# Kernel tuning notes

Measured on AMD Instinct MI355X. Metric: run time of the kernel, lower is better.

## Reference

```python
import jax, jax.numpy as jnp
import numpy as np

N_SRC1, N_DST1, N_DST2 = 200000, 50000, 10000
E1, E2 = 2000000, 400000
IN_F, H_F, N_CLS = 128, 256, 47


def setup_inputs() -> dict:
    key = jax.random.key(0)
    ks = jax.random.split(key, 10)
    x = jax.random.normal(ks[0], (N_SRC1, IN_F), dtype=jnp.float32)
    W_self1 = jax.random.normal(ks[1], (IN_F, H_F), dtype=jnp.float32) * (1.0 / np.sqrt(IN_F))
    W_neigh1 = jax.random.normal(ks[2], (IN_F, H_F), dtype=jnp.float32) * (1.0 / np.sqrt(IN_F))
    b1 = jnp.zeros((H_F,), dtype=jnp.float32)
    W_self2 = jax.random.normal(ks[3], (H_F, N_CLS), dtype=jnp.float32) * (1.0 / np.sqrt(H_F))
    W_neigh2 = jax.random.normal(ks[4], (H_F, N_CLS), dtype=jnp.float32) * (1.0 / np.sqrt(H_F))
    b2 = jnp.zeros((N_CLS,), dtype=jnp.float32)
    src1 = jax.random.randint(ks[5], (E1,), 0, N_SRC1, dtype=jnp.int64)
    dst1 = jnp.sort(jax.random.randint(ks[6], (E1,), 0, N_DST1, dtype=jnp.int64))
    src2 = jax.random.randint(ks[7], (E2,), 0, N_DST1, dtype=jnp.int64)
    dst2 = jnp.sort(jax.random.randint(ks[8], (E2,), 0, N_DST2, dtype=jnp.int64))
    return {"x": x, "W_self1": W_self1, "W_neigh1": W_neigh1, "b1": b1,
            "W_self2": W_self2, "W_neigh2": W_neigh2, "b2": b2,
            "src1": src1, "dst1": dst1, "src2": src2, "dst2": dst2,
            "n_dst1": N_DST1, "n_dst2": N_DST2}


def _sage_mean(h_src, h_dst, src, dst, n_dst, W_self, W_neigh, b):
    # mean neighbor aggregation: gather src feats, segment-sum onto dst, divide by in-degree
    msum = jax.ops.segment_sum(h_src[src], dst, num_segments=n_dst)  # [n_dst, F]
    deg = jax.ops.segment_sum(jnp.ones(src.shape, h_src.dtype), dst, num_segments=n_dst)
    h_neigh = msum / jnp.maximum(deg, 1.0)[:, None]
    return h_dst @ W_self + h_neigh @ W_neigh + b


def reference(x, W_self1, W_neigh1, b1, W_self2, W_neigh2, b2,
              src1, dst1, src2, dst2, n_dst1, n_dst2):
    # layer 1 (dst nodes are the prefix of src nodes, DGL MFG convention)
    h = _sage_mean(x, x[:n_dst1], src1, dst1, n_dst1, W_self1, W_neigh1, b1)
    h = jax.nn.relu(h)  # dropout = identity (eval mode)
    # layer 2
    out = _sage_mean(h, h[:n_dst2], src2, dst2, n_dst2, W_self2, W_neigh2, b2)
    return out
```

## Files before the change

### kernel.cpp

```cpp
#include <hip/hip_runtime.h>

constexpr int N_DST1 = 50000;
constexpr int N_DST2 = 10000;
constexpr int E1     = 2000000;
constexpr int E2     = 400000;
constexpr int IN_F   = 128;
constexpr int H_F    = 256;
constexpr int N_CLS  = 47;

constexpr size_t RP1_OFF = 0;
constexpr size_t RP2_OFF = 204800;
constexpr size_t BPS_OFF = 245760;
constexpr size_t BPN_OFF = 311296;
constexpr size_t BP2_OFF = 376832;
constexpr size_t X8_OFF  = 430080;
constexpr size_t HN1_OFF = 26030080;
constexpr size_t HB_OFF  = 38830080;
constexpr size_t H8_OFF  = 64430080;
constexpr size_t HN2_OFF = 77230080;

using f32x4  = __attribute__((ext_vector_type(4))) float;
using f32x2  = __attribute__((ext_vector_type(2))) float;
using short8 = __attribute__((ext_vector_type(8))) short;

__device__ __forceinline__ ushort f2bf(float f) {
    union { float f; unsigned u; } v; v.f = f;
    unsigned u = v.u;
    return (ushort)((u + 0x7fffu + ((u >> 16) & 1u)) >> 16);
}

constexpr int CAST_BLKS = 200000 * IN_F / 8 / 256;
constexpr int PACK_BLKS = 44;
constexpr int RP_BLKS   = (N_DST1 + N_DST2 + 2 + 255) / 256;

__global__ __launch_bounds__(256) void setup_all(
    const float* __restrict__ x, unsigned char* __restrict__ x8,
    const float* __restrict__ Ws1, const float* __restrict__ Wn1,
    const float* __restrict__ Ws2, const float* __restrict__ Wn2,
    ushort* __restrict__ bps, ushort* __restrict__ bpn, ushort* __restrict__ bp2,
    const int* __restrict__ dst1, const int* __restrict__ dst2,
    int* __restrict__ rp1, int* __restrict__ rp2) {
    int b = blockIdx.x;
    if (b < CAST_BLKS) {
        int i = b * 256 + threadIdx.x;
        float4 v0 = ((const float4*)x)[2 * i];
        float4 v1 = ((const float4*)x)[2 * i + 1];
        int p0 = __builtin_amdgcn_cvt_pk_fp8_f32(v0.x, v0.y, 0, false);
        p0     = __builtin_amdgcn_cvt_pk_fp8_f32(v0.z, v0.w, p0, true);
        int p1 = __builtin_amdgcn_cvt_pk_fp8_f32(v1.x, v1.y, 0, false);
        p1     = __builtin_amdgcn_cvt_pk_fp8_f32(v1.z, v1.w, p1, true);
        uint2 o; o.x = (unsigned)p0; o.y = (unsigned)p1;
        ((uint2*)x8)[i] = o;
    } else if (b < CAST_BLKS + PACK_BLKS) {
        int pb = b - CAST_BLKS;
        if (pb < 32) {
            const float* W = (pb < 16) ? Ws1 : Wn1;
            ushort* P      = (pb < 16) ? bps : bpn;
            int idx = (pb & 15) * 256 + threadIdx.x;
            int lane = idx & 63, kb = (idx >> 6) & 3, nb = idx >> 8;
            int n  = nb * 16 + (lane & 15);
            int k0 = kb * 32 + ((lane >> 4) * 8);
            ushort tmp[8];
#pragma unroll
            for (int j = 0; j < 8; ++j) tmp[j] = f2bf(W[(k0 + j) * H_F + n]);
            ((uint4*)P)[idx] = *(uint4*)tmp;
        } else {
            int idx = (pb - 32) * 256 + threadIdx.x;
            if (idx < 3072) {
                int lane = idx & 63, rem = idx >> 6;
                int nb = rem % 3, kb = rem / 3;
                int col = nb * 16 + (lane & 15);
                int k0  = (kb & 7) * 32 + ((lane >> 4) * 8);
                const float* W = (kb < 8) ? Ws2 : Wn2;
                ushort tmp[8];
#pragma unroll
                for (int j = 0; j < 8; ++j)
                    tmp[j] = (col < N_CLS) ? f2bf(W[(k0 + j) * N_CLS + col]) : (ushort)0;
                ((uint4*)bp2)[(kb * 3 + nb) * 64 + lane] = *(uint4*)tmp;
            }
        }
    } else {
        int idx = (b - CAST_BLKS - PACK_BLKS) * 256 + threadIdx.x;
        const int* dst; int* rp; int E; int target;
        if (idx <= N_DST1) { dst = dst1; rp = rp1; E = E1; target = idx; }
        else if (idx <= N_DST1 + 1 + N_DST2) {
            dst = dst2; rp = rp2; E = E2; target = idx - (N_DST1 + 1);
        } else return;
        int lo = 0, hi = E;
        while (lo < hi) {
            int mid = (lo + hi) >> 1;
            if (dst[mid] < target) lo = mid + 1; else hi = mid;
        }
        rp[target] = lo;
    }
}

__global__ __launch_bounds__(256) void agg1b(const unsigned char* __restrict__ x8,
                                             const int* __restrict__ src,
                                             const int* __restrict__ rp,
                                             ushort* __restrict__ hn) {
    int t = threadIdx.x & 63;
    int d = blockIdx.x * 4 + (threadIdx.x >> 6);
    int s = rp[d], e = rp[d + 1];
    int deg = e - s;
    const uint4* x4 = (const uint4*)x8;
    int g = t >> 3, c = t & 7;
    float a[16] = {};
    auto acc16 = [&](uint4 v) {
        f32x2 f;
        f = __builtin_amdgcn_cvt_pk_f32_fp8((int)v.x, false); a[0]  += f[0]; a[1]  += f[1];
        f = __builtin_amdgcn_cvt_pk_f32_fp8((int)v.x, true);  a[2]  += f[0]; a[3]  += f[1];
        f = __builtin_amdgcn_cvt_pk_f32_fp8((int)v.y, false); a[4]  += f[0]; a[5]  += f[1];
        f = __builtin_amdgcn_cvt_pk_f32_fp8((int)v.y, true);  a[6]  += f[0]; a[7]  += f[1];
        f = __builtin_amdgcn_cvt_pk_f32_fp8((int)v.z, false); a[8]  += f[0]; a[9]  += f[1];
        f = __builtin_amdgcn_cvt_pk_f32_fp8((int)v.z, true);  a[10] += f[0]; a[11] += f[1];
        f = __builtin_amdgcn_cvt_pk_f32_fp8((int)v.w, false); a[12] += f[0]; a[13] += f[1];
        f = __builtin_amdgcn_cvt_pk_f32_fp8((int)v.w, true);  a[14] += f[0]; a[15] += f[1];
    };
    int nfull = deg >> 3;
    int j = 0;
    for (; j + 2 <= nfull; j += 2) {
        int e0 = src[s + 8 * j + g];
        int e1 = src[s + 8 * j + 8 + g];
        uint4 v0 = x4[(size_t)e0 * 8 + c];
        uint4 v1 = x4[(size_t)e1 * 8 + c];
        acc16(v0);
        acc16(v1);
    }
    for (; j < nfull; ++j) {
        int e0 = src[s + 8 * j + g];
        uint4 v = x4[(size_t)e0 * 8 + c];
        acc16(v);
    }
    int b0 = s + 8 * nfull;
    int n = e - b0;
    if (g < n) {
        int e0 = src[b0 + g];
        uint4 v = x4[(size_t)e0 * 8 + c];
        acc16(v);
    }
#pragma unroll
    for (int q = 0; q < 16; ++q) {
        a[q] += __shfl_xor(a[q], 8);
        a[q] += __shfl_xor(a[q], 16);
        a[q] += __shfl_xor(a[q], 32);
    }
    if (t < 8) {
        float inv = 1.f / fmaxf((float)deg, 1.f);
        unsigned o[8];
#pragma unroll
        for (int p = 0; p < 8; ++p)
            o[p] = (unsigned)f2bf(a[2 * p] * inv) |
                   ((unsigned)f2bf(a[2 * p + 1] * inv) << 16);
        uint4* hrow = (uint4*)hn + (size_t)d * 16 + t * 2;
        hrow[0] = make_uint4(o[0], o[1], o[2], o[3]);
        hrow[1] = make_uint4(o[4], o[5], o[6], o[7]);
    }
}

__global__ __launch_bounds__(256) void agg2b(const unsigned char* __restrict__ h8,
                                             const int* __restrict__ src,
                                             const int* __restrict__ rp,
                                             ushort* __restrict__ hn) {
    int t = threadIdx.x & 63;
    int d = blockIdx.x * 4 + (threadIdx.x >> 6);
    int s = rp[d], e = rp[d + 1];
    int deg = e - s;
    const uint4* h4 = (const uint4*)h8;
    int g = t >> 4, c = t & 15;
    float a[16] = {};
    auto acc16 = [&](uint4 v) {
        f32x2 f;
        f = __builtin_amdgcn_cvt_pk_f32_fp8((int)v.x, false); a[0]  += f[0]; a[1]  += f[1];
        f = __builtin_amdgcn_cvt_pk_f32_fp8((int)v.x, true);  a[2]  += f[0]; a[3]  += f[1];
        f = __builtin_amdgcn_cvt_pk_f32_fp8((int)v.y, false); a[4]  += f[0]; a[5]  += f[1];
        f = __builtin_amdgcn_cvt_pk_f32_fp8((int)v.y, true);  a[6]  += f[0]; a[7]  += f[1];
        f = __builtin_amdgcn_cvt_pk_f32_fp8((int)v.z, false); a[8]  += f[0]; a[9]  += f[1];
        f = __builtin_amdgcn_cvt_pk_f32_fp8((int)v.z, true);  a[10] += f[0]; a[11] += f[1];
        f = __builtin_amdgcn_cvt_pk_f32_fp8((int)v.w, false); a[12] += f[0]; a[13] += f[1];
        f = __builtin_amdgcn_cvt_pk_f32_fp8((int)v.w, true);  a[14] += f[0]; a[15] += f[1];
    };
    int nfull = deg >> 2;
    int j = 0;
    for (; j + 2 <= nfull; j += 2) {
        int e0 = src[s + 4 * j + g];
        int e1 = src[s + 4 * j + 4 + g];
        uint4 v0 = h4[(size_t)e0 * 16 + c];
        uint4 v1 = h4[(size_t)e1 * 16 + c];
        acc16(v0);
        acc16(v1);
    }
    for (; j < nfull; ++j) {
        int e0 = src[s + 4 * j + g];
        uint4 v = h4[(size_t)e0 * 16 + c];
        acc16(v);
    }
    int b0 = s + 4 * nfull;
    int n = e - b0;
    if (g < n) {
        int e0 = src[b0 + g];
        uint4 v = h4[(size_t)e0 * 16 + c];
        acc16(v);
    }
#pragma unroll
    for (int q = 0; q < 16; ++q) {
        a[q] += __shfl_xor(a[q], 16);
        a[q] += __shfl_xor(a[q], 32);
    }
    if (t < 16) {
        float inv = 1.f / fmaxf((float)deg, 1.f);
        unsigned o[8];
#pragma unroll
        for (int p = 0; p < 8; ++p)
            o[p] = (unsigned)f2bf(a[2 * p] * inv) |
                   ((unsigned)f2bf(a[2 * p + 1] * inv) << 16);
        uint4* hrow = (uint4*)hn + (size_t)d * 32 + t * 2;
        hrow[0] = make_uint4(o[0], o[1], o[2], o[3]);
        hrow[1] = make_uint4(o[4], o[5], o[6], o[7]);
    }
}

__global__ __launch_bounds__(256) void gemm1_mfma(
    const float* __restrict__ x, const ushort* __restrict__ hn1,
    const ushort* __restrict__ BpS, const ushort* __restrict__ BpN,
    const float* __restrict__ b1, ushort* __restrict__ hb,
    unsigned char* __restrict__ h8) {
    int tid = threadIdx.x;
    int wave = tid >> 6, lane = tid & 63;
    int m0 = blockIdx.x * 16;
    int nb0 = wave * 4;
    int mloc = lane & 15;
    int mrow = m0 + mloc;
    int koff = (lane >> 4) * 8;

    const float*  Af = x   + (size_t)mrow * IN_F;
    const ushort* Ah = hn1 + (size_t)mrow * IN_F;
    short8 a0[4], a1[4];
#pragma unroll
    for (int kb = 0; kb < 4; ++kb) {
        float4 q0 = *(const float4*)(Af + kb * 32 + koff);
        float4 q1 = *(const float4*)(Af + kb * 32 + koff + 4);
        a0[kb][0] = (short)f2bf(q0.x); a0[kb][1] = (short)f2bf(q0.y);
        a0[kb][2] = (short)f2bf(q0.z); a0[kb][3] = (short)f2bf(q0.w);
        a0[kb][4] = (short)f2bf(q1.x); a0[kb][5] = (short)f2bf(q1.y);
        a0[kb][6] = (short)f2bf(q1.z); a0[kb][7] = (short)f2bf(q1.w);
        a1[kb] = *(const short8*)(Ah + kb * 32 + koff);
    }

    f32x4 acc[4];
#pragma unroll
    for (int nb = 0; nb < 4; ++nb) acc[nb] = (f32x4){0.f, 0.f, 0.f, 0.f};

#pragma unroll
    for (int kb = 0; kb < 4; ++kb)
#pragma unroll
        for (int nb = 0; nb < 4; ++nb) {
            short8 b = *(const short8*)(BpS + ((size_t)((nb0 + nb) * 4 + kb) * 64 + lane) * 8);
            acc[nb] = __builtin_amdgcn_mfma_f32_16x16x32_bf16(a0[kb], b, acc[nb], 0, 0, 0);
        }
#pragma unroll
    for (int kb = 0; kb < 4; ++kb)
#pragma unroll
        for (int nb = 0; nb < 4; ++nb) {
            short8 b = *(const short8*)(BpN + ((size_t)((nb0 + nb) * 4 + kb) * 64 + lane) * 8);
            acc[nb] = __builtin_amdgcn_mfma_f32_16x16x32_bf16(a1[kb], b, acc[nb], 0, 0, 0);
        }

    int crow0 = m0 + (lane >> 4) * 4;
    int ccol  = lane & 15;
#pragma unroll
    for (int nb = 0; nb < 4; ++nb) {
        size_t col = (size_t)(nb0 + nb) * 16 + ccol;
        float bias = b1[col];
#pragma unroll
        for (int r = 0; r < 4; ++r) {
            int row = crow0 + r;
            float v = fmaxf(acc[nb][r] + bias, 0.f);
            int p = __builtin_amdgcn_cvt_pk_fp8_f32(v, v, 0, false);
            h8[(size_t)row * H_F + col] = (unsigned char)(p & 0xff);
            if (row < N_DST2) hb[(size_t)row * H_F + col] = f2bf(v);
        }
    }
}

__global__ __launch_bounds__(256) void gemm2_mfma(
    const ushort* __restrict__ hb, const ushort* __restrict__ hn2,
    const ushort* __restrict__ P2, const float* __restrict__ b2,
    float* __restrict__ out) {
    int tid = threadIdx.x;
    int wave = tid >> 6, lane = tid & 63;
    int m0 = (blockIdx.x * 4 + wave) * 16;
    if (m0 >= N_DST2) return;
    int mrow = m0 + (lane & 15);
    int koff = (lane >> 4) * 8;

    f32x4 acc[3];
#pragma unroll
    for (int nb = 0; nb < 3; ++nb) acc[nb] = (f32x4){0.f, 0.f, 0.f, 0.f};

#pragma unroll
    for (int kb = 0; kb < 16; ++kb) {
        const ushort* A = (kb < 8)
            ? (hb  + (size_t)mrow * H_F + kb * 32 + koff)
            : (hn2 + (size_t)mrow * H_F + (kb - 8) * 32 + koff);
        short8 a = *(const short8*)A;
#pragma unroll
        for (int nb = 0; nb < 3; ++nb) {
            short8 b = *(const short8*)(P2 + ((size_t)(kb * 3 + nb) * 64 + lane) * 8);
            acc[nb] = __builtin_amdgcn_mfma_f32_16x16x32_bf16(a, b, acc[nb], 0, 0, 0);
        }
    }
    int crow0 = m0 + (lane >> 4) * 4;
    int ccol  = lane & 15;
#pragma unroll
    for (int nb = 0; nb < 3; ++nb) {
        int col = nb * 16 + ccol;
        if (col < N_CLS) {
            float bias = b2[col];
#pragma unroll
            for (int r = 0; r < 4; ++r)
                out[(size_t)(crow0 + r) * N_CLS + col] = acc[nb][r] + bias;
        }
    }
}

extern "C" void kernel_launch(void* const* d_in, const int* in_sizes, int n_in,
                              void* d_out, int out_size, void* d_ws, size_t ws_size,
                              hipStream_t stream) {
    const float* x   = (const float*)d_in[0];
    const float* Ws1 = (const float*)d_in[1];
    const float* Wn1 = (const float*)d_in[2];
    const float* b1  = (const float*)d_in[3];
    const float* Ws2 = (const float*)d_in[4];
    const float* Wn2 = (const float*)d_in[5];
    const float* b2  = (const float*)d_in[6];
    const int* src1  = (const int*)d_in[7];
    const int* dst1  = (const int*)d_in[8];
    const int* src2  = (const int*)d_in[9];
    const int* dst2  = (const int*)d_in[10];
    float* out = (float*)d_out;

    char* ws = (char*)d_ws;
    int*           rp1 = (int*)(ws + RP1_OFF);
    int*           rp2 = (int*)(ws + RP2_OFF);
    ushort*        bps = (ushort*)(ws + BPS_OFF);
    ushort*        bpn = (ushort*)(ws + BPN_OFF);
    ushort*        bp2 = (ushort*)(ws + BP2_OFF);
    unsigned char* x8  = (unsigned char*)(ws + X8_OFF);
    ushort*        hn1 = (ushort*)(ws + HN1_OFF);
    ushort*        hb  = (ushort*)(ws + HB_OFF);
    unsigned char* h8  = (unsigned char*)(ws + H8_OFF);
    ushort*        hn2 = (ushort*)(ws + HN2_OFF);

    setup_all<<<CAST_BLKS + PACK_BLKS + RP_BLKS, 256, 0, stream>>>(
        x, x8, Ws1, Wn1, Ws2, Wn2, bps, bpn, bp2, dst1, dst2, rp1, rp2);
    agg1b<<<N_DST1 / 4, 256, 0, stream>>>(x8, src1, rp1, hn1);
    gemm1_mfma<<<N_DST1 / 16, 256, 0, stream>>>(x, hn1, bps, bpn, b1, hb, h8);
    agg2b<<<N_DST2 / 4, 256, 0, stream>>>(h8, src2, rp2, hn2);
    gemm2_mfma<<<(N_DST2 / 16 + 3) / 4, 256, 0, stream>>>(hb, hn2, bp2, b2, out);
}
```

Before: 287.6 us.

## Fuse neighbor aggregation into GEMM kernels via LDS staging, split-K in layer two

```diff
diff --git a/kernel.cpp b/kernel.cpp
--- a/kernel.cpp
+++ b/kernel.cpp
@@ -14,10 +14,8 @@
 constexpr size_t BPN_OFF = 311296;
 constexpr size_t BP2_OFF = 376832;
 constexpr size_t X8_OFF  = 430080;
-constexpr size_t HN1_OFF = 26030080;
 constexpr size_t HB_OFF  = 38830080;
 constexpr size_t H8_OFF  = 64430080;
-constexpr size_t HN2_OFF = 77230080;
 
 using f32x4  = __attribute__((ext_vector_type(4))) float;
 using f32x2  = __attribute__((ext_vector_type(2))) float;
@@ -95,146 +93,85 @@
     }
 }
 
-__global__ __launch_bounds__(256) void agg1b(const unsigned char* __restrict__ x8,
-                                             const int* __restrict__ src,
-                                             const int* __restrict__ rp,
-                                             ushort* __restrict__ hn) {
-    int t = threadIdx.x & 63;
-    int d = blockIdx.x * 4 + (threadIdx.x >> 6);
-    int s = rp[d], e = rp[d + 1];
-    int deg = e - s;
-    const uint4* x4 = (const uint4*)x8;
-    int g = t >> 3, c = t & 7;
-    float a[16] = {};
-    auto acc16 = [&](uint4 v) {
-        f32x2 f;
-        f = __builtin_amdgcn_cvt_pk_f32_fp8((int)v.x, false); a[0]  += f[0]; a[1]  += f[1];
-        f = __builtin_amdgcn_cvt_pk_f32_fp8((int)v.x, true);  a[2]  += f[0]; a[3]  += f[1];
-        f = __builtin_amdgcn_cvt_pk_f32_fp8((int)v.y, false); a[4]  += f[0]; a[5]  += f[1];
-        f = __builtin_amdgcn_cvt_pk_f32_fp8((int)v.y, true);  a[6]  += f[0]; a[7]  += f[1];
-        f = __builtin_amdgcn_cvt_pk_f32_fp8((int)v.z, false); a[8]  += f[0]; a[9]  += f[1];
-        f = __builtin_amdgcn_cvt_pk_f32_fp8((int)v.z, true);  a[10] += f[0]; a[11] += f[1];
-        f = __builtin_amdgcn_cvt_pk_f32_fp8((int)v.w, false); a[12] += f[0]; a[13] += f[1];
-        f = __builtin_amdgcn_cvt_pk_f32_fp8((int)v.w, true);  a[14] += f[0]; a[15] += f[1];
-    };
-    int nfull = deg >> 3;
-    int j = 0;
-    for (; j + 2 <= nfull; j += 2) {
-        int e0 = src[s + 8 * j + g];
-        int e1 = src[s + 8 * j + 8 + g];
-        uint4 v0 = x4[(size_t)e0 * 8 + c];
-        uint4 v1 = x4[(size_t)e1 * 8 + c];
-        acc16(v0);
-        acc16(v1);
-    }
-    for (; j < nfull; ++j) {
-        int e0 = src[s + 8 * j + g];
-        uint4 v = x4[(size_t)e0 * 8 + c];
-        acc16(v);
-    }
-    int b0 = s + 8 * nfull;
-    int n = e - b0;
-    if (g < n) {
-        int e0 = src[b0 + g];
-        uint4 v = x4[(size_t)e0 * 8 + c];
-        acc16(v);
-    }
-#pragma unroll
-    for (int q = 0; q < 16; ++q) {
-        a[q] += __shfl_xor(a[q], 8);
-        a[q] += __shfl_xor(a[q], 16);
-        a[q] += __shfl_xor(a[q], 32);
-    }
-    if (t < 8) {
-        float inv = 1.f / fmaxf((float)deg, 1.f);
-        unsigned o[8];
-#pragma unroll
-        for (int p = 0; p < 8; ++p)
-            o[p] = (unsigned)f2bf(a[2 * p] * inv) |
-                   ((unsigned)f2bf(a[2 * p + 1] * inv) << 16);
-        uint4* hrow = (uint4*)hn + (size_t)d * 16 + t * 2;
-        hrow[0] = make_uint4(o[0], o[1], o[2], o[3]);
-        hrow[1] = make_uint4(o[4], o[5], o[6], o[7]);
-    }
-}
-
-__global__ __launch_bounds__(256) void agg2b(const unsigned char* __restrict__ h8,
-                                             const int* __restrict__ src,
-                                             const int* __restrict__ rp,
-                                             ushort* __restrict__ hn) {
-    int t = threadIdx.x & 63;
-    int d = blockIdx.x * 4 + (threadIdx.x >> 6);
-    int s = rp[d], e = rp[d + 1];
-    int deg = e - s;
-    const uint4* h4 = (const uint4*)h8;
-    int g = t >> 4, c = t & 15;
-    float a[16] = {};
-    auto acc16 = [&](uint4 v) {
-        f32x2 f;
-        f = __builtin_amdgcn_cvt_pk_f32_fp8((int)v.x, false); a[0]  += f[0]; a[1]  += f[1];
-        f = __builtin_amdgcn_cvt_pk_f32_fp8((int)v.x, true);  a[2]  += f[0]; a[3]  += f[1];
-        f = __builtin_amdgcn_cvt_pk_f32_fp8((int)v.y, false); a[4]  += f[0]; a[5]  += f[1];
-        f = __builtin_amdgcn_cvt_pk_f32_fp8((int)v.y, true);  a[6]  += f[0]; a[7]  += f[1];
-        f = __builtin_amdgcn_cvt_pk_f32_fp8((int)v.z, false); a[8]  += f[0]; a[9]  += f[1];
-        f = __builtin_amdgcn_cvt_pk_f32_fp8((int)v.z, true);  a[10] += f[0]; a[11] += f[1];
-        f = __builtin_amdgcn_cvt_pk_f32_fp8((int)v.w, false); a[12] += f[0]; a[13] += f[1];
-        f = __builtin_amdgcn_cvt_pk_f32_fp8((int)v.w, true);  a[14] += f[0]; a[15] += f[1];
-    };
-    int nfull = deg >> 2;
-    int j = 0;
-    for (; j + 2 <= nfull; j += 2) {
-        int e0 = src[s + 4 * j + g];
-        int e1 = src[s + 4 * j + 4 + g];
-        uint4 v0 = h4[(size_t)e0 * 16 + c];
-        uint4 v1 = h4[(size_t)e1 * 16 + c];
-        acc16(v0);
-        acc16(v1);
-    }
-    for (; j < nfull; ++j) {
-        int e0 = src[s + 4 * j + g];
-        uint4 v = h4[(size_t)e0 * 16 + c];
-        acc16(v);
-    }
-    int b0 = s + 4 * nfull;
-    int n = e - b0;
-    if (g < n) {
-        int e0 = src[b0 + g];
-        uint4 v = h4[(size_t)e0 * 16 + c];
-        acc16(v);
-    }
-#pragma unroll
-    for (int q = 0; q < 16; ++q) {
-        a[q] += __shfl_xor(a[q], 16);
-        a[q] += __shfl_xor(a[q], 32);
-    }
-    if (t < 16) {
-        float inv = 1.f / fmaxf((float)deg, 1.f);
-        unsigned o[8];
-#pragma unroll
-        for (int p = 0; p < 8; ++p)
-            o[p] = (unsigned)f2bf(a[2 * p] * inv) |
-                   ((unsigned)f2bf(a[2 * p + 1] * inv) << 16);
-        uint4* hrow = (uint4*)hn + (size_t)d * 32 + t * 2;
-        hrow[0] = make_uint4(o[0], o[1], o[2], o[3]);
-        hrow[1] = make_uint4(o[4], o[5], o[6], o[7]);
-    }
-}
-
-__global__ __launch_bounds__(256) void gemm1_mfma(
-    const float* __restrict__ x, const ushort* __restrict__ hn1,
+__global__ __launch_bounds__(256, 4) void fused1(
+    const unsigned char* __restrict__ x8, const int* __restrict__ src,
+    const int* __restrict__ rp, const float* __restrict__ x,
     const ushort* __restrict__ BpS, const ushort* __restrict__ BpN,
     const float* __restrict__ b1, ushort* __restrict__ hb,
     unsigned char* __restrict__ h8) {
+    __shared__ ushort lhn[16][136];
     int tid = threadIdx.x;
     int wave = tid >> 6, lane = tid & 63;
     int m0 = blockIdx.x * 16;
+
+    const uint4* x4 = (const uint4*)x8;
+    int g = lane >> 3, c = lane & 7;
+#pragma unroll 1
+    for (int q = 0; q < 4; ++q) {
+        int row = wave * 4 + q;
+        int d = m0 + row;
+        int s = rp[d], e = rp[d + 1];
+        int deg = e - s;
+        float a[16] = {};
+        auto acc16 = [&](uint4 v) {
+            f32x2 f;
+            f = __builtin_amdgcn_cvt_pk_f32_fp8((int)v.x, false); a[0]  += f[0]; a[1]  += f[1];
+            f = __builtin_amdgcn_cvt_pk_f32_fp8((int)v.x, true);  a[2]  += f[0]; a[3]  += f[1];
+            f = __builtin_amdgcn_cvt_pk_f32_fp8((int)v.y, false); a[4]  += f[0]; a[5]  += f[1];
+            f = __builtin_amdgcn_cvt_pk_f32_fp8((int)v.y, true);  a[6]  += f[0]; a[7]  += f[1];
+            f = __builtin_amdgcn_cvt_pk_f32_fp8((int)v.z, false); a[8]  += f[0]; a[9]  += f[1];
+            f = __builtin_amdgcn_cvt_pk_f32_fp8((int)v.z, true);  a[10] += f[0]; a[11] += f[1];
+            f = __builtin_amdgcn_cvt_pk_f32_fp8((int)v.w, false); a[12] += f[0]; a[13] += f[1];
+            f = __builtin_amdgcn_cvt_pk_f32_fp8((int)v.w, true);  a[14] += f[0]; a[15] += f[1];
+        };
+        int nfull = deg >> 3;
+        int j = 0;
+        for (; j + 2 <= nfull; j += 2) {
+            int e0 = src[s + 8 * j + g];
+            int e1 = src[s + 8 * j + 8 + g];
+            uint4 v0 = x4[(size_t)e0 * 8 + c];
+            uint4 v1 = x4[(size_t)e1 * 8 + c];
+            acc16(v0);
+            acc16(v1);
+        }
+        for (; j < nfull; ++j) {
+            int e0 = src[s + 8 * j + g];
+            uint4 v = x4[(size_t)e0 * 8 + c];
+            acc16(v);
+        }
+        int b0 = s + 8 * nfull;
+        int n = e - b0;
+        if (g < n) {
+            int e0 = src[b0 + g];
+            uint4 v = x4[(size_t)e0 * 8 + c];
+            acc16(v);
+        }
+#pragma unroll
+        for (int qq = 0; qq < 16; ++qq) {
+            a[qq] += __shfl_xor(a[qq], 8);
+            a[qq] += __shfl_xor(a[qq], 16);
+            a[qq] += __shfl_xor(a[qq], 32);
+        }
+        if (lane < 8) {
+            float inv = 1.f / fmaxf((float)deg, 1.f);
+            unsigned o[8];
+#pragma unroll
+            for (int p = 0; p < 8; ++p)
+                o[p] = (unsigned)f2bf(a[2 * p] * inv) |
+                       ((unsigned)f2bf(a[2 * p + 1] * inv) << 16);
+            uint4* dp = (uint4*)&lhn[row][lane * 16];
+            dp[0] = make_uint4(o[0], o[1], o[2], o[3]);
+            dp[1] = make_uint4(o[4], o[5], o[6], o[7]);
+        }
+    }
+    __syncthreads();
+
     int nb0 = wave * 4;
     int mloc = lane & 15;
     int mrow = m0 + mloc;
     int koff = (lane >> 4) * 8;
 
-    const float*  Af = x   + (size_t)mrow * IN_F;
-    const ushort* Ah = hn1 + (size_t)mrow * IN_F;
+    const float* Af = x + (size_t)mrow * IN_F;
     short8 a0[4], a1[4];
 #pragma unroll
     for (int kb = 0; kb < 4; ++kb) {
@@ -244,7 +181,7 @@
         a0[kb][2] = (short)f2bf(q0.z); a0[kb][3] = (short)f2bf(q0.w);
         a0[kb][4] = (short)f2bf(q1.x); a0[kb][5] = (short)f2bf(q1.y);
         a0[kb][6] = (short)f2bf(q1.z); a0[kb][7] = (short)f2bf(q1.w);
-        a1[kb] = *(const short8*)(Ah + kb * 32 + koff);
+        a1[kb] = *(const short8*)&lhn[mloc][kb * 32 + koff];
     }
 
     f32x4 acc[4];
@@ -283,15 +220,80 @@
     }
 }
 
-__global__ __launch_bounds__(256) void gemm2_mfma(
-    const ushort* __restrict__ hb, const ushort* __restrict__ hn2,
+__global__ __launch_bounds__(256, 4) void fused2(
+    const unsigned char* __restrict__ h8, const int* __restrict__ src,
+    const int* __restrict__ rp, const ushort* __restrict__ hb,
     const ushort* __restrict__ P2, const float* __restrict__ b2,
     float* __restrict__ out) {
+    __shared__ ushort lhn[16][264];
+    __shared__ float lred[3][3][64][4];
     int tid = threadIdx.x;
     int wave = tid >> 6, lane = tid & 63;
-    int m0 = (blockIdx.x * 4 + wave) * 16;
-    if (m0 >= N_DST2) return;
-    int mrow = m0 + (lane & 15);
+    int m0 = blockIdx.x * 16;
+
+    const uint4* h4 = (const uint4*)h8;
+    int g = lane >> 4, c = lane & 15;
+#pragma unroll 1
+    for (int q = 0; q < 4; ++q) {
+        int row = wave * 4 + q;
+        int d = m0 + row;
+        int s = rp[d], e = rp[d + 1];
+        int deg = e - s;
+        float a[16] = {};
+        auto acc16 = [&](uint4 v) {
+            f32x2 f;
+            f = __builtin_amdgcn_cvt_pk_f32_fp8((int)v.x, false); a[0]  += f[0]; a[1]  += f[1];
+            f = __builtin_amdgcn_cvt_pk_f32_fp8((int)v.x, true);  a[2]  += f[0]; a[3]  += f[1];
+            f = __builtin_amdgcn_cvt_pk_f32_fp8((int)v.y, false); a[4]  += f[0]; a[5]  += f[1];
+            f = __builtin_amdgcn_cvt_pk_f32_fp8((int)v.y, true);  a[6]  += f[0]; a[7]  += f[1];
+            f = __builtin_amdgcn_cvt_pk_f32_fp8((int)v.z, false); a[8]  += f[0]; a[9]  += f[1];
+            f = __builtin_amdgcn_cvt_pk_f32_fp8((int)v.z, true);  a[10] += f[0]; a[11] += f[1];
+            f = __builtin_amdgcn_cvt_pk_f32_fp8((int)v.w, false); a[12] += f[0]; a[13] += f[1];
+            f = __builtin_amdgcn_cvt_pk_f32_fp8((int)v.w, true);  a[14] += f[0]; a[15] += f[1];
+        };
+        int nfull = deg >> 2;
+        int j = 0;
+        for (; j + 2 <= nfull; j += 2) {
+            int e0 = src[s + 4 * j + g];
+            int e1 = src[s + 4 * j + 4 + g];
+            uint4 v0 = h4[(size_t)e0 * 16 + c];
+            uint4 v1 = h4[(size_t)e1 * 16 + c];
+            acc16(v0);
+            acc16(v1);
+        }
+        for (; j < nfull; ++j) {
+            int e0 = src[s + 4 * j + g];
+            uint4 v = h4[(size_t)e0 * 16 + c];
+            acc16(v);
+        }
+        int b0 = s + 4 * nfull;
+        int n = e - b0;
+        if (g < n) {
+            int e0 = src[b0 + g];
+            uint4 v = h4[(size_t)e0 * 16 + c];
+            acc16(v);
+        }
+#pragma unroll
+        for (int qq = 0; qq < 16; ++qq) {
+            a[qq] += __shfl_xor(a[qq], 16);
+            a[qq] += __shfl_xor(a[qq], 32);
+        }
+        if (lane < 16) {
+            float inv = 1.f / fmaxf((float)deg, 1.f);
+            unsigned o[8];
+#pragma unroll
+            for (int p = 0; p < 8; ++p)
+                o[p] = (unsigned)f2bf(a[2 * p] * inv) |
+                       ((unsigned)f2bf(a[2 * p + 1] * inv) << 16);
+            uint4* dp = (uint4*)&lhn[row][lane * 16];
+            dp[0] = make_uint4(o[0], o[1], o[2], o[3]);
+            dp[1] = make_uint4(o[4], o[5], o[6], o[7]);
+        }
+    }
+    __syncthreads();
+
+    int mloc = lane & 15;
+    int mrow = m0 + mloc;
     int koff = (lane >> 4) * 8;
 
     f32x4 acc[3];
@@ -299,27 +301,44 @@
     for (int nb = 0; nb < 3; ++nb) acc[nb] = (f32x4){0.f, 0.f, 0.f, 0.f};
 
 #pragma unroll
-    for (int kb = 0; kb < 16; ++kb) {
-        const ushort* A = (kb < 8)
-            ? (hb  + (size_t)mrow * H_F + kb * 32 + koff)
-            : (hn2 + (size_t)mrow * H_F + (kb - 8) * 32 + koff);
-        short8 a = *(const short8*)A;
+    for (int i = 0; i < 4; ++i) {
+        int kb = wave * 4 + i;
+        short8 a;
+        if (wave < 2)
+            a = *(const short8*)(hb + (size_t)mrow * H_F + kb * 32 + koff);
+        else
+            a = *(const short8*)&lhn[mloc][(kb - 8) * 32 + koff];
 #pragma unroll
         for (int nb = 0; nb < 3; ++nb) {
             short8 b = *(const short8*)(P2 + ((size_t)(kb * 3 + nb) * 64 + lane) * 8);
             acc[nb] = __builtin_amdgcn_mfma_f32_16x16x32_bf16(a, b, acc[nb], 0, 0, 0);
         }
     }
-    int crow0 = m0 + (lane >> 4) * 4;
-    int ccol  = lane & 15;
-#pragma unroll
-    for (int nb = 0; nb < 3; ++nb) {
-        int col = nb * 16 + ccol;
-        if (col < N_CLS) {
-            float bias = b2[col];
+
+    if (wave != 0) {
+#pragma unroll
+        for (int nb = 0; nb < 3; ++nb)
 #pragma unroll
             for (int r = 0; r < 4; ++r)
-                out[(size_t)(crow0 + r) * N_CLS + col] = acc[nb][r] + bias;
+                lred[wave - 1][nb][lane][r] = acc[nb][r];
+    }
+    __syncthreads();
+    if (wave == 0) {
+        int crow0 = m0 + (lane >> 4) * 4;
+        int ccol  = lane & 15;
+#pragma unroll
+        for (int nb = 0; nb < 3; ++nb) {
+            int col = nb * 16 + ccol;
+#pragma unroll
+            for (int r = 0; r < 4; ++r)
+                acc[nb][r] += lred[0][nb][lane][r] + lred[1][nb][lane][r] +
+                              lred[2][nb][lane][r];
+            if (col < N_CLS) {
+                float bias = b2[col];
+#pragma unroll
+                for (int r = 0; r < 4; ++r)
+                    out[(size_t)(crow0 + r) * N_CLS + col] = acc[nb][r] + bias;
+            }
         }
     }
 }
@@ -347,15 +366,11 @@
     ushort*        bpn = (ushort*)(ws + BPN_OFF);
     ushort*        bp2 = (ushort*)(ws + BP2_OFF);
     unsigned char* x8  = (unsigned char*)(ws + X8_OFF);
-    ushort*        hn1 = (ushort*)(ws + HN1_OFF);
     ushort*        hb  = (ushort*)(ws + HB_OFF);
     unsigned char* h8  = (unsigned char*)(ws + H8_OFF);
-    ushort*        hn2 = (ushort*)(ws + HN2_OFF);
 
     setup_all<<<CAST_BLKS + PACK_BLKS + RP_BLKS, 256, 0, stream>>>(
         x, x8, Ws1, Wn1, Ws2, Wn2, bps, bpn, bp2, dst1, dst2, rp1, rp2);
-    agg1b<<<N_DST1 / 4, 256, 0, stream>>>(x8, src1, rp1, hn1);
-    gemm1_mfma<<<N_DST1 / 16, 256, 0, stream>>>(x, hn1, bps, bpn, b1, hb, h8);
-    agg2b<<<N_DST2 / 4, 256, 0, stream>>>(h8, src2, rp2, hn2);
-    gemm2_mfma<<<(N_DST2 / 16 + 3) / 4, 256, 0, stream>>>(hb, hn2, bp2, b2, out);
-}
+    fused1<<<N_DST1 / 16, 256, 0, stream>>>(x8, src1, rp1, x, bps, bpn, b1, hb, h8);
+    fused2<<<N_DST2 / 16, 256, 0, stream>>>(h8, src2, rp2, hb, bp2, b2, out);
+}
```

New measurement: 310.9 us. 8.1% more time.
